# Kernel tuning notes

Hardware: AMD Instinct MI355X
Metric: run time of the kernel (lower is better)

The kernel has to match this reference:

```python
import jax, jax.numpy as jnp
import numpy as np

EMBED = 1024

def setup_inputs() -> dict:
    key = jax.random.key(0)
    ks = jax.random.split(key, 7)
    s = 1.0 / np.sqrt(EMBED)
    x = jax.random.normal(ks[0], (8, 2048, EMBED), dtype=jnp.float32)
    Wk = jax.random.uniform(ks[1], (EMBED, EMBED), jnp.float32, -s, s)
    bk = jax.random.uniform(ks[2], (EMBED,), jnp.float32, -s, s)
    Wq = jax.random.uniform(ks[3], (EMBED, EMBED), jnp.float32, -s, s)
    bq = jax.random.uniform(ks[4], (EMBED,), jnp.float32, -s, s)
    Wv = jax.random.uniform(ks[5], (EMBED, EMBED), jnp.float32, -s, s)
    bv = jax.random.uniform(ks[6], (EMBED,), jnp.float32, -s, s)
    return {"x": x, "Wq": Wq, "bq": bq, "Wk": Wk, "bk": bk, "Wv": Wv, "bv": bv}

def reference(x, Wq, bq, Wk, bk, Wv, bv):
    # Linear projections (PyTorch Linear: y = x @ W^T + b; W here stored as [in, out] = W^T)
    Q = x @ Wq + bq          # [b, s, d]
    K = x @ Wk + bk
    V = x @ Wv + bv
    scale = 1.0 / jnp.sqrt(jnp.asarray(x.shape[-1], x.dtype))
    scores = jnp.einsum('bqd,bkd->bqk', Q, K) * scale  # [b, s, s]
    attn = jax.nn.softmax(scores, axis=-1)
    return jnp.einsum('bqk,bkd->bqd', attn, V)
```

## Files before the change

### kernel.cpp

```cpp
#include <hip/hip_runtime.h>

typedef __attribute__((ext_vector_type(4))) float f32x4;
typedef __attribute__((ext_vector_type(8))) short bf16x8;
typedef __attribute__((ext_vector_type(4))) unsigned short u16x4;

static __device__ __forceinline__ unsigned short f2bf(float f) {
    union { float f; unsigned int u; } a; a.f = f;
    unsigned int u = a.u;
    unsigned int r = (u + 0x7FFFu + ((u >> 16) & 1u)) >> 16;
    return (unsigned short)r;
}
static __device__ __forceinline__ float bf2f(unsigned short h) {
    union { unsigned int u; float f; } a; a.u = ((unsigned int)h) << 16;
    return a.f;
}
static __device__ __forceinline__ unsigned lds_off(const void* p) {
    return (unsigned)(unsigned long long)(const __attribute__((address_space(3))) void*)p;
}

__global__ __launch_bounds__(256) void cvt_f32_bf16(const float* __restrict__ in,
                                                    unsigned short* __restrict__ out) {
    long long i = ((long long)blockIdx.x * 256 + threadIdx.x) * 4;
    float4 f = *(const float4*)(in + i);
    u16x4 u;
    u[0] = f2bf(f.x); u[1] = f2bf(f.y); u[2] = f2bf(f.z); u[3] = f2bf(f.w);
    *(u16x4*)(out + i) = u;
}

__global__ __launch_bounds__(256) void transpose_w(const float* __restrict__ W0,
                                                   const float* __restrict__ W1,
                                                   const float* __restrict__ W2,
                                                   unsigned short* __restrict__ Wt) {
    __shared__ float t[32][33];
    int mat = blockIdx.z;
    const float* W = (mat == 0) ? W0 : (mat == 1) ? W1 : W2;
    unsigned short* out = Wt + (long long)mat * 1024 * 1024;
    int n0 = blockIdx.x * 32, k0 = blockIdx.y * 32;
    int tx = threadIdx.x, ty = threadIdx.y;
#pragma unroll
    for (int q = 0; q < 4; ++q)
        t[ty + 8 * q][tx] = W[(long long)(k0 + ty + 8 * q) * 1024 + n0 + tx];
    __syncthreads();
#pragma unroll
    for (int q = 0; q < 4; ++q)
        out[(long long)(n0 + ty + 8 * q) * 1024 + k0 + tx] = f2bf(t[tx][ty + 8 * q]);
}

#define GBM 256
#define GBN 256
#define GBK 64

template<int OUT_MODE, int BIAS_MODE>
__global__ __launch_bounds__(512, 2) void gemm8p(
    const unsigned short* __restrict__ A, int lda, long long strideA,
    const unsigned short* __restrict__ B, int ldb, long long strideB,
    void* __restrict__ Cv, int ldc, long long strideC,
    const float* __restrict__ bias, int K, float scale)
{
    __shared__ __align__(16) unsigned short As[2][GBM * GBK];
    __shared__ __align__(16) unsigned short Bs[2][GBN * GBK];

    const int gx = gridDim.x, gy = gridDim.y;
    int lin = blockIdx.x + gx * (blockIdx.y + gy * blockIdx.z);
    const int nwg = gx * gy * gridDim.z;
    const int qch = nwg >> 3;
    int swz = (lin & 7) * qch + (lin >> 3);
    const int bx = swz % gx; int t2 = swz / gx;
    const int by = t2 % gy;  const int bz = t2 / gy;

    const unsigned short* Ag = A + (long long)bz * strideA;
    const unsigned short* Bg = B + (long long)bz * strideB;
    const int m0 = by * GBM, n0 = bx * GBN;

    const int tid  = threadIdx.x;
    const int lane = tid & 63, w = tid >> 6;
    const int wm = w >> 2, wn = w & 3;
    const int l15 = lane & 15, l4 = lane >> 4;

    const int sg = (lane & 7) ^ ((lane >> 3) & 7);
    const unsigned short* Asrc = Ag + (long long)(m0 + w * 8 + (lane >> 3)) * lda + sg * 8;
    const unsigned short* Bsrc = Bg + (long long)(n0 + w * 8 + (lane >> 3)) * ldb + sg * 8;

    f32x4 acc[8][4] = {};

    auto issueA = [&](int p, int kt, int l) {
        __builtin_amdgcn_global_load_lds(
            (const __attribute__((address_space(1))) void*)(Asrc + (long long)(l * 64) * lda + kt),
            (__attribute__((address_space(3))) void*)(&As[p][(l * 64 + w * 8) * GBK]), 16, 0, 0);
    };
    auto issueB = [&](int p, int kt, int l) {
        __builtin_amdgcn_global_load_lds(
            (const __attribute__((address_space(1))) void*)(Bsrc + (long long)(l * 64) * ldb + kt),
            (__attribute__((address_space(3))) void*)(&Bs[p][(l * 64 + w * 8) * GBK]), 16, 0, 0);
    };
    auto readA = [&](bf16x8 (&af)[4], int p, int mh, int ks) {
#pragma unroll
        for (int fi = 0; fi < 4; ++fi) {
            int ar = wm * 128 + mh * 64 + fi * 16 + l15;
            int slot = (ks * 4 + l4) ^ (ar & 7);
            unsigned off = lds_off(&As[p][ar * GBK + slot * 8]);
            asm volatile("ds_read_b128 %0, %1" : "=v"(af[fi]) : "v"(off));
        }
    };
    auto readB = [&](bf16x8 (&bf)[4], int p, int ks) {
#pragma unroll
        for (int nj = 0; nj < 4; ++nj) {
            int br = wn * 64 + nj * 16 + l15;
            int slot = (ks * 4 + l4) ^ (br & 7);
            unsigned off = lds_off(&Bs[p][br * GBK + slot * 8]);
            asm volatile("ds_read_b128 %0, %1" : "=v"(bf[nj]) : "v"(off));
        }
    };
    auto mfma16 = [&](int mh, bf16x8 (&af)[4], bf16x8 (&bf)[4]) {
#pragma unroll
        for (int fi = 0; fi < 4; ++fi)
#pragma unroll
            for (int nj = 0; nj < 4; ++nj)
                acc[mh * 4 + fi][nj] = __builtin_amdgcn_mfma_f32_16x16x32_bf16(
                    af[fi], bf[nj], acc[mh * 4 + fi][nj], 0, 0, 0);
    };

#define VMCNT2 asm volatile("s_waitcnt vmcnt(2)" ::: "memory")
#define VMCNT0 asm volatile("s_waitcnt vmcnt(0)" ::: "memory")
#define LGKM0  asm volatile("s_waitcnt lgkmcnt(0)" ::: "memory")
#define SCHED0 __builtin_amdgcn_sched_barrier(0)
#define BARR   __builtin_amdgcn_s_barrier()
#define PRIO1  __builtin_amdgcn_s_setprio(1)
#define PRIO0  __builtin_amdgcn_s_setprio(0)

    issueB(0, 0, 0); issueB(0, 0, 1); issueB(0, 0, 2); issueB(0, 0, 3);
    issueA(0, 0, 0); issueA(0, 0, 2); issueA(0, 0, 1); issueA(0, 0, 3);

    const int NT = K >> 6;
    bf16x8 a0[4], a1[4], b0[4], b1[4];

    for (int t = 0; t < NT - 1; ++t) {
        const int p = t & 1, q = p ^ 1;
        const int kn = (t + 1) << 6;
        VMCNT2; BARR; SCHED0;
        issueB(q, kn, 0); issueB(q, kn, 1);
        readA(a0, p, 0, 0); readB(b0, p, 0);
        LGKM0; SCHED0; PRIO1; mfma16(0, a0, b0); PRIO0;
        VMCNT2; BARR; SCHED0;
        issueB(q, kn, 2); issueB(q, kn, 3);
        readA(a1, p, 1, 0);
        LGKM0; SCHED0; PRIO1; mfma16(1, a1, b0); PRIO0;
        issueA(q, kn, 0); issueA(q, kn, 2);
        readA(a0, p, 0, 1); readB(b1, p, 1);
        LGKM0; SCHED0; PRIO1; mfma16(0, a0, b1); PRIO0;
        issueA(q, kn, 1); issueA(q, kn, 3);
        readA(a1, p, 1, 1);
        LGKM0; SCHED0; PRIO1; mfma16(1, a1, b1); PRIO0;
    }
    {
        const int p = (NT - 1) & 1;
        VMCNT0; BARR; SCHED0;
        readA(a0, p, 0, 0); readB(b0, p, 0);
        LGKM0; SCHED0; PRIO1; mfma16(0, a0, b0); PRIO0;
        readA(a1, p, 1, 0);
        LGKM0; SCHED0; PRIO1; mfma16(1, a1, b0); PRIO0;
        readA(a0, p, 0, 1); readB(b1, p, 1);
        LGKM0; SCHED0; PRIO1; mfma16(0, a0, b1); PRIO0;
        readA(a1, p, 1, 1);
        LGKM0; SCHED0; PRIO1; mfma16(1, a1, b1); PRIO0;
    }

    const float* bias_v = bias;
    asm volatile("" : "+s"(bias_v));
    unsigned short* Cb = (unsigned short*)Cv;
    float* Cf = (float*)Cv;
    long long cbase = (long long)bz * strideC;
#pragma unroll
    for (int mh = 0; mh < 2; ++mh)
#pragma unroll
    for (int fi = 0; fi < 4; ++fi) {
#pragma unroll
        for (int nj = 0; nj < 4; ++nj) {
            int n = n0 + wn * 64 + nj * 16 + l15;
            float bn = (BIAS_MODE == 1) ? bias_v[n] : 0.0f;
#pragma unroll
            for (int r = 0; r < 4; ++r) {
                int m = m0 + wm * 128 + mh * 64 + fi * 16 + l4 * 4 + r;
                float v = acc[mh * 4 + fi][nj][r] * scale + bn;
                if (BIAS_MODE == 2) v += bias_v[m];
                long long idx = cbase + (long long)m * ldc + n;
                if (OUT_MODE == 0) Cb[idx] = f2bf(v);
                else               Cf[idx] = v;
            }
        }
    }
}

__global__ __launch_bounds__(256) void softmax_rows_bf16(unsigned short* __restrict__ S) {
    int row  = blockIdx.x * 4 + (threadIdx.x >> 6);
    int lane = threadIdx.x & 63;
    unsigned short* Srow = S + (long long)row * 2048;
    float v[32];
    float mx = -1e30f;
#pragma unroll
    for (int j = 0; j < 4; ++j) {
        bf16x8 h = *(const bf16x8*)(Srow + j * 512 + lane * 8);
#pragma unroll
        for (int e = 0; e < 8; ++e) {
            float f = bf2f((unsigned short)h[e]);
            v[j * 8 + e] = f;
            mx = fmaxf(mx, f);
        }
    }
#pragma unroll
    for (int o = 32; o; o >>= 1) mx = fmaxf(mx, __shfl_xor(mx, o));
    float sum = 0.0f;
#pragma unroll
    for (int e = 0; e < 32; ++e) {
        v[e] = __expf(v[e] - mx);
        sum += v[e];
    }
#pragma unroll
    for (int o = 32; o; o >>= 1) sum += __shfl_xor(sum, o);
    float inv = 1.0f / sum;
#pragma unroll
    for (int j = 0; j < 4; ++j) {
        bf16x8 h;
#pragma unroll
        for (int e = 0; e < 8; ++e) h[e] = (short)f2bf(v[j * 8 + e] * inv);
        *(bf16x8*)(Srow + j * 512 + lane * 8) = h;
    }
}

extern "C" void kernel_launch(void* const* d_in, const int* in_sizes, int n_in,
                              void* d_out, int out_size, void* d_ws, size_t ws_size,
                              hipStream_t stream) {
    (void)in_sizes; (void)n_in; (void)out_size; (void)ws_size;
    const float* x  = (const float*)d_in[0];
    const float* Wq = (const float*)d_in[1];
    const float* bq = (const float*)d_in[2];
    const float* Wk = (const float*)d_in[3];
    const float* bk = (const float*)d_in[4];
    const float* Wv = (const float*)d_in[5];
    const float* bv = (const float*)d_in[6];

    char* ws = (char*)d_ws;
    unsigned short* Wt  = (unsigned short*)ws;
    unsigned short* Qb  = (unsigned short*)(ws + 6291456);
    unsigned short* Kb  = (unsigned short*)(ws + 39845888);
    unsigned short* Vt  = (unsigned short*)(ws + 73400320);
    unsigned short* xb  = (unsigned short*)(ws + 106954752);
    unsigned short* Sb  = (unsigned short*)(ws + 106954752);

    cvt_f32_bf16<<<dim3(16384), dim3(256), 0, stream>>>(x, xb);
    transpose_w<<<dim3(32, 32, 3), dim3(32, 8), 0, stream>>>(Wq, Wk, Wv, Wt);

    gemm8p<0, 1><<<dim3(4, 64, 1), dim3(512), 0, stream>>>(
        xb, 1024, 0, Wt, 1024, 0, Qb, 1024, 0, bq, 1024, 1.0f);
    gemm8p<0, 1><<<dim3(4, 64, 1), dim3(512), 0, stream>>>(
        xb, 1024, 0, Wt + 1048576, 1024, 0, Kb, 1024, 0, bk, 1024, 1.0f);
    gemm8p<0, 2><<<dim3(64, 4, 1), dim3(512), 0, stream>>>(
        Wt + 2097152, 1024, 0, xb, 1024, 0, Vt, 16384, 0, bv, 1024, 1.0f);

    gemm8p<0, 0><<<dim3(8, 8, 8), dim3(512), 0, stream>>>(
        Qb, 1024, 2097152LL, Kb, 1024, 2097152LL,
        Sb, 2048, 4194304LL, nullptr, 1024, 0.03125f);

    softmax_rows_bf16<<<dim3(4096), dim3(256), 0, stream>>>(Sb);

    gemm8p<1, 0><<<dim3(4, 8, 8), dim3(512), 0, stream>>>(
        Sb, 2048, 4194304LL,
        Vt, 16384, 2048LL,
        d_out, 1024, 2097152LL, nullptr, 2048, 1.0f);
}
```

Baseline: 269.7 us.

## Switch GEMM to 4-stage K=32 LDS ring buffer with deeper prefetch

Replaces the double-buffered K=64 tile pipeline with a four-slot ring of K=32 tiles in a single 128KB LDS array, keeping three tiles in flight ahead of compute. The swizzle changes to a 4-slot XOR pattern and LDS read addresses are precomputed as constant offsets, which cuts per-read address arithmetic. The aim is to hide global-load latency better and cut barrier stalls. In exchange there are twice as many barriers per K, and 128KB of LDS per block may limit occupancy to fewer blocks than the launch bound of two.

Result: slower. 288.2 us (+6.9%).

```diff
diff --git a/kernel.cpp b/kernel.cpp
--- a/kernel.cpp
+++ b/kernel.cpp
@@ -48,17 +48,15 @@
 
 #define GBM 256
 #define GBN 256
-#define GBK 64
 
 template<int OUT_MODE, int BIAS_MODE>
-__global__ __launch_bounds__(512, 2) void gemm8p(
+__global__ __launch_bounds__(512, 2) void gemm4b(
     const unsigned short* __restrict__ A, int lda, long long strideA,
     const unsigned short* __restrict__ B, int ldb, long long strideB,
     void* __restrict__ Cv, int ldc, long long strideC,
     const float* __restrict__ bias, int K, float scale)
 {
-    __shared__ __align__(16) unsigned short As[2][GBM * GBK];
-    __shared__ __align__(16) unsigned short Bs[2][GBN * GBK];
+    __shared__ __align__(16) char lds[131072];
 
     const int gx = gridDim.x, gy = gridDim.y;
     int lin = blockIdx.x + gx * (blockIdx.y + gy * blockIdx.z);
@@ -77,37 +75,41 @@
     const int wm = w >> 2, wn = w & 3;
     const int l15 = lane & 15, l4 = lane >> 4;
 
-    const int sg = (lane & 7) ^ ((lane >> 3) & 7);
-    const unsigned short* Asrc = Ag + (long long)(m0 + w * 8 + (lane >> 3)) * lda + sg * 8;
-    const unsigned short* Bsrc = Bg + (long long)(n0 + w * 8 + (lane >> 3)) * ldb + sg * 8;
+    const int lr  = lane >> 2;
+    const int lsl = (lane & 3) ^ (lr & 3);
+    const unsigned short* Asrc = Ag + (long long)(m0 + w * 16 + lr) * lda + lsl * 8;
+    const unsigned short* Bsrc = Bg + (long long)(n0 + w * 16 + lr) * ldb + lsl * 8;
 
     f32x4 acc[8][4] = {};
 
-    auto issueA = [&](int p, int kt, int l) {
+    auto issueA = [&](int wb, int kt, int l) {
         __builtin_amdgcn_global_load_lds(
-            (const __attribute__((address_space(1))) void*)(Asrc + (long long)(l * 64) * lda + kt),
-            (__attribute__((address_space(3))) void*)(&As[p][(l * 64 + w * 8) * GBK]), 16, 0, 0);
-    };
-    auto issueB = [&](int p, int kt, int l) {
+            (const __attribute__((address_space(1))) void*)(Asrc + (long long)(l * 128) * lda + kt),
+            (__attribute__((address_space(3))) void*)(lds + wb + (l * 128 + w * 16) * 64), 16, 0, 0);
+    };
+    auto issueB = [&](int wb, int kt, int l) {
         __builtin_amdgcn_global_load_lds(
-            (const __attribute__((address_space(1))) void*)(Bsrc + (long long)(l * 64) * ldb + kt),
-            (__attribute__((address_space(3))) void*)(&Bs[p][(l * 64 + w * 8) * GBK]), 16, 0, 0);
-    };
-    auto readA = [&](bf16x8 (&af)[4], int p, int mh, int ks) {
+            (const __attribute__((address_space(1))) void*)(Bsrc + (long long)(l * 128) * ldb + kt),
+            (__attribute__((address_space(3))) void*)(lds + 65536 + wb + (l * 128 + w * 16) * 64), 16, 0, 0);
+    };
+
+    const unsigned ldsb  = lds_off(lds);
+    const unsigned slotb = (unsigned)((l4 ^ (l15 & 3)) * 16);
+    const unsigned aoffc = ldsb + (unsigned)((wm * 128 + l15) * 64) + slotb;
+    const unsigned boffc = ldsb + 65536u + (unsigned)((wn * 64 + l15) * 64) + slotb;
+
+    bf16x8 a0[4], a1[4], b0[4];
+    auto readA = [&](bf16x8 (&af)[4], int rb, int mh) {
 #pragma unroll
         for (int fi = 0; fi < 4; ++fi) {
-            int ar = wm * 128 + mh * 64 + fi * 16 + l15;
-            int slot = (ks * 4 + l4) ^ (ar & 7);
-            unsigned off = lds_off(&As[p][ar * GBK + slot * 8]);
+            unsigned off = aoffc + rb + mh * 4096 + fi * 1024;
             asm volatile("ds_read_b128 %0, %1" : "=v"(af[fi]) : "v"(off));
         }
     };
-    auto readB = [&](bf16x8 (&bf)[4], int p, int ks) {
+    auto readB = [&](bf16x8 (&bf)[4], int rb) {
 #pragma unroll
         for (int nj = 0; nj < 4; ++nj) {
-            int br = wn * 64 + nj * 16 + l15;
-            int slot = (ks * 4 + l4) ^ (br & 7);
-            unsigned off = lds_off(&Bs[p][br * GBK + slot * 8]);
+            unsigned off = boffc + rb + nj * 1024;
             asm volatile("ds_read_b128 %0, %1" : "=v"(bf[nj]) : "v"(off));
         }
     };
@@ -120,7 +122,8 @@
                     af[fi], bf[nj], acc[mh * 4 + fi][nj], 0, 0, 0);
     };
 
-#define VMCNT2 asm volatile("s_waitcnt vmcnt(2)" ::: "memory")
+#define VMCNT8 asm volatile("s_waitcnt vmcnt(8)" ::: "memory")
+#define VMCNT4 asm volatile("s_waitcnt vmcnt(4)" ::: "memory")
 #define VMCNT0 asm volatile("s_waitcnt vmcnt(0)" ::: "memory")
 #define LGKM0  asm volatile("s_waitcnt lgkmcnt(0)" ::: "memory")
 #define SCHED0 __builtin_amdgcn_sched_barrier(0)
@@ -128,41 +131,42 @@
 #define PRIO1  __builtin_amdgcn_s_setprio(1)
 #define PRIO0  __builtin_amdgcn_s_setprio(0)
 
-    issueB(0, 0, 0); issueB(0, 0, 1); issueB(0, 0, 2); issueB(0, 0, 3);
-    issueA(0, 0, 0); issueA(0, 0, 2); issueA(0, 0, 1); issueA(0, 0, 3);
-
-    const int NT = K >> 6;
-    bf16x8 a0[4], a1[4], b0[4], b1[4];
-
-    for (int t = 0; t < NT - 1; ++t) {
-        const int p = t & 1, q = p ^ 1;
-        const int kn = (t + 1) << 6;
-        VMCNT2; BARR; SCHED0;
-        issueB(q, kn, 0); issueB(q, kn, 1);
-        readA(a0, p, 0, 0); readB(b0, p, 0);
+    const int NT = K >> 5;
+#pragma unroll
+    for (int t = 0; t < 3; ++t) {
+        int wb = t * 16384, kt = t * 32;
+        issueA(wb, kt, 0); issueA(wb, kt, 1);
+        issueB(wb, kt, 0); issueB(wb, kt, 1);
+    }
+
+    int rb = 0;
+    for (int t = 0; t < NT - 2; ++t) {
+        VMCNT8; BARR; SCHED0;
+        const int kt3 = (t + 3) * 32;
+        const int wb = (rb + 49152) & 65535;
+        const bool more = (t + 3) < NT;
+        if (more) { issueA(wb, kt3, 0); issueA(wb, kt3, 1); }
+        readB(b0, rb); readA(a0, rb, 0);
         LGKM0; SCHED0; PRIO1; mfma16(0, a0, b0); PRIO0;
-        VMCNT2; BARR; SCHED0;
-        issueB(q, kn, 2); issueB(q, kn, 3);
-        readA(a1, p, 1, 0);
+        if (more) { issueB(wb, kt3, 0); issueB(wb, kt3, 1); }
+        readA(a1, rb, 1);
         LGKM0; SCHED0; PRIO1; mfma16(1, a1, b0); PRIO0;
-        issueA(q, kn, 0); issueA(q, kn, 2);
-        readA(a0, p, 0, 1); readB(b1, p, 1);
-        LGKM0; SCHED0; PRIO1; mfma16(0, a0, b1); PRIO0;
-        issueA(q, kn, 1); issueA(q, kn, 3);
-        readA(a1, p, 1, 1);
-        LGKM0; SCHED0; PRIO1; mfma16(1, a1, b1); PRIO0;
+        rb = (rb + 16384) & 65535;
     }
     {
-        const int p = (NT - 1) & 1;
+        VMCNT4; BARR; SCHED0;
+        readB(b0, rb); readA(a0, rb, 0);
+        LGKM0; SCHED0; PRIO1; mfma16(0, a0, b0); PRIO0;
+        readA(a1, rb, 1);
+        LGKM0; SCHED0; PRIO1; mfma16(1, a1, b0); PRIO0;
+        rb = (rb + 16384) & 65535;
+    }
+    {
         VMCNT0; BARR; SCHED0;
-        readA(a0, p, 0, 0); readB(b0, p, 0);
+        readB(b0, rb); readA(a0, rb, 0);
         LGKM0; SCHED0; PRIO1; mfma16(0, a0, b0); PRIO0;
-        readA(a1, p, 1, 0);
+        readA(a1, rb, 1);
         LGKM0; SCHED0; PRIO1; mfma16(1, a1, b0); PRIO0;
-        readA(a0, p, 0, 1); readB(b1, p, 1);
-        LGKM0; SCHED0; PRIO1; mfma16(0, a0, b1); PRIO0;
-        readA(a1, p, 1, 1);
-        LGKM0; SCHED0; PRIO1; mfma16(1, a1, b1); PRIO0;
     }
 
     const float* bias_v = bias;
@@ -250,20 +254,20 @@
     cvt_f32_bf16<<<dim3(16384), dim3(256), 0, stream>>>(x, xb);
     transpose_w<<<dim3(32, 32, 3), dim3(32, 8), 0, stream>>>(Wq, Wk, Wv, Wt);
 
-    gemm8p<0, 1><<<dim3(4, 64, 1), dim3(512), 0, stream>>>(
+    gemm4b<0, 1><<<dim3(4, 64, 1), dim3(512), 0, stream>>>(
         xb, 1024, 0, Wt, 1024, 0, Qb, 1024, 0, bq, 1024, 1.0f);
-    gemm8p<0, 1><<<dim3(4, 64, 1), dim3(512), 0, stream>>>(
+    gemm4b<0, 1><<<dim3(4, 64, 1), dim3(512), 0, stream>>>(
         xb, 1024, 0, Wt + 1048576, 1024, 0, Kb, 1024, 0, bk, 1024, 1.0f);
-    gemm8p<0, 2><<<dim3(64, 4, 1), dim3(512), 0, stream>>>(
+    gemm4b<0, 2><<<dim3(64, 4, 1), dim3(512), 0, stream>>>(
         Wt + 2097152, 1024, 0, xb, 1024, 0, Vt, 16384, 0, bv, 1024, 1.0f);
 
-    gemm8p<0, 0><<<dim3(8, 8, 8), dim3(512), 0, stream>>>(
+    gemm4b<0, 0><<<dim3(8, 8, 8), dim3(512), 0, stream>>>(
         Qb, 1024, 2097152LL, Kb, 1024, 2097152LL,
         Sb, 2048, 4194304LL, nullptr, 1024, 0.03125f);
 
     softmax_rows_bf16<<<dim3(4096), dim3(256), 0, stream>>>(Sb);
 
-    gemm8p<1, 0><<<dim3(4, 8, 8), dim3(512), 0, stream>>>(
+    gemm4b<1, 0><<<dim3(4, 8, 8), dim3(512), 0, stream>>>(
         Sb, 2048, 4194304LL,
         Vt, 16384, 2048LL,
         d_out, 1024, 2097152LL, nullptr, 2048, 1.0f);
```

## Restructure GEMM main loop into half-tile staged prefetch with per-phase barriers

Applied to the files above, without the earlier changes.

Replaces the separate A/B shared arrays with one raw LDS buffer and precomputes swizzled read offsets so each LDS read is a base plus a constant stride. The K-loop is reorganized so each MFMA phase is bracketed by barriers and the next tile's A/B halves are staged in finer pieces, with the first A half of tile t+2 prefetched into the buffer being consumed. The peeled epilogue iteration is folded in via guards. The goal is better overlap of global-to-LDS loads with MFMA work and cheaper address arithmetic, at the cost of many more barriers per iteration and tighter buffer-reuse hazards.

New measurement: 285.8 us. 1.06x slower.

```diff
diff --git a/kernel.cpp b/kernel.cpp
--- a/kernel.cpp
+++ b/kernel.cpp
@@ -48,7 +48,6 @@
 
 #define GBM 256
 #define GBN 256
-#define GBK 64
 
 template<int OUT_MODE, int BIAS_MODE>
 __global__ __launch_bounds__(512, 2) void gemm8p(
@@ -57,8 +56,7 @@
     void* __restrict__ Cv, int ldc, long long strideC,
     const float* __restrict__ bias, int K, float scale)
 {
-    __shared__ __align__(16) unsigned short As[2][GBM * GBK];
-    __shared__ __align__(16) unsigned short Bs[2][GBN * GBK];
+    __shared__ __align__(16) char lds[131072];
 
     const int gx = gridDim.x, gy = gridDim.y;
     int lin = blockIdx.x + gx * (blockIdx.y + gy * blockIdx.z);
@@ -77,37 +75,48 @@
     const int wm = w >> 2, wn = w & 3;
     const int l15 = lane & 15, l4 = lane >> 4;
 
-    const int sg = (lane & 7) ^ ((lane >> 3) & 7);
-    const unsigned short* Asrc = Ag + (long long)(m0 + w * 8 + (lane >> 3)) * lda + sg * 8;
-    const unsigned short* Bsrc = Bg + (long long)(n0 + w * 8 + (lane >> 3)) * ldb + sg * 8;
+    const int sr = lane >> 3;
+    const int ss = (lane & 7) ^ sr;
+    const unsigned short* Asrc = Ag + (long long)(m0 + w * 8 + sr) * lda + ss * 8;
+    const unsigned short* Bsrc = Bg + (long long)(n0 + w * 8 + sr) * ldb + ss * 8;
 
     f32x4 acc[8][4] = {};
 
-    auto issueA = [&](int p, int kt, int l) {
-        __builtin_amdgcn_global_load_lds(
-            (const __attribute__((address_space(1))) void*)(Asrc + (long long)(l * 64) * lda + kt),
-            (__attribute__((address_space(3))) void*)(&As[p][(l * 64 + w * 8) * GBK]), 16, 0, 0);
-    };
-    auto issueB = [&](int p, int kt, int l) {
-        __builtin_amdgcn_global_load_lds(
-            (const __attribute__((address_space(1))) void*)(Bsrc + (long long)(l * 64) * ldb + kt),
-            (__attribute__((address_space(3))) void*)(&Bs[p][(l * 64 + w * 8) * GBK]), 16, 0, 0);
-    };
+    auto stageA = [&](int p, int kt, int h) {
+#pragma unroll
+        for (int i = 0; i < 2; ++i)
+            __builtin_amdgcn_global_load_lds(
+                (const __attribute__((address_space(1))) void*)(Asrc + (long long)(h * 128 + i * 64) * lda + kt),
+                (__attribute__((address_space(3))) void*)(lds + p * 32768 + (h * 128 + i * 64 + w * 8) * 128), 16, 0, 0);
+    };
+    auto stageB = [&](int p, int kt, int h) {
+#pragma unroll
+        for (int i = 0; i < 2; ++i)
+            __builtin_amdgcn_global_load_lds(
+                (const __attribute__((address_space(1))) void*)(Bsrc + (long long)(h * 128 + i * 64) * ldb + kt),
+                (__attribute__((address_space(3))) void*)(lds + 65536 + p * 32768 + (h * 128 + i * 64 + w * 8) * 128), 16, 0, 0);
+    };
+
+    const unsigned ldsb = lds_off(lds);
+    const unsigned as0  = (unsigned)(((l4    ) ^ (l15 & 7)) * 16);
+    const unsigned as1  = (unsigned)(((l4 + 4) ^ (l15 & 7)) * 16);
+    const unsigned aRow = (unsigned)((wm * 128 + l15) * 128);
+    const unsigned bRow = (unsigned)((wn * 64 + l15) * 128);
+
+    bf16x8 a0[4], a1[4], b0[4], b1[4];
     auto readA = [&](bf16x8 (&af)[4], int p, int mh, int ks) {
+        unsigned base = ldsb + (unsigned)(p * 32768) + aRow + (unsigned)(mh * 8192) + (ks ? as1 : as0);
 #pragma unroll
         for (int fi = 0; fi < 4; ++fi) {
-            int ar = wm * 128 + mh * 64 + fi * 16 + l15;
-            int slot = (ks * 4 + l4) ^ (ar & 7);
-            unsigned off = lds_off(&As[p][ar * GBK + slot * 8]);
+            unsigned off = base + (unsigned)(fi * 2048);
             asm volatile("ds_read_b128 %0, %1" : "=v"(af[fi]) : "v"(off));
         }
     };
     auto readB = [&](bf16x8 (&bf)[4], int p, int ks) {
+        unsigned base = ldsb + 65536u + (unsigned)(p * 32768) + bRow + (ks ? as1 : as0);
 #pragma unroll
         for (int nj = 0; nj < 4; ++nj) {
-            int br = wn * 64 + nj * 16 + l15;
-            int slot = (ks * 4 + l4) ^ (br & 7);
-            unsigned off = lds_off(&Bs[p][br * GBK + slot * 8]);
+            unsigned off = base + (unsigned)(nj * 2048);
             asm volatile("ds_read_b128 %0, %1" : "=v"(bf[nj]) : "v"(off));
         }
     };
@@ -128,41 +137,28 @@
 #define PRIO1  __builtin_amdgcn_s_setprio(1)
 #define PRIO0  __builtin_amdgcn_s_setprio(0)
 
-    issueB(0, 0, 0); issueB(0, 0, 1); issueB(0, 0, 2); issueB(0, 0, 3);
-    issueA(0, 0, 0); issueA(0, 0, 2); issueA(0, 0, 1); issueA(0, 0, 3);
-
     const int NT = K >> 6;
-    bf16x8 a0[4], a1[4], b0[4], b1[4];
-
-    for (int t = 0; t < NT - 1; ++t) {
+    stageA(0, 0, 0); stageA(0, 0, 1); stageB(0, 0, 0); stageB(0, 0, 1);
+    stageA(1, 64, 0);
+    VMCNT2; BARR; SCHED0;
+
+    for (int t = 0; t < NT; ++t) {
         const int p = t & 1, q = p ^ 1;
-        const int kn = (t + 1) << 6;
-        VMCNT2; BARR; SCHED0;
-        issueB(q, kn, 0); issueB(q, kn, 1);
+        const int kt1 = (t + 1) << 6, kt2 = (t + 2) << 6;
+        const bool s1 = (t + 1) < NT, s2 = (t + 2) < NT;
         readA(a0, p, 0, 0); readB(b0, p, 0);
-        LGKM0; SCHED0; PRIO1; mfma16(0, a0, b0); PRIO0;
-        VMCNT2; BARR; SCHED0;
-        issueB(q, kn, 2); issueB(q, kn, 3);
+        if (s1) stageB(q, kt1, 0);
+        BARR; LGKM0; SCHED0; PRIO1; mfma16(0, a0, b0); PRIO0; BARR;
         readA(a1, p, 1, 0);
-        LGKM0; SCHED0; PRIO1; mfma16(1, a1, b0); PRIO0;
-        issueA(q, kn, 0); issueA(q, kn, 2);
+        if (s1) stageA(q, kt1, 1);
+        BARR; LGKM0; SCHED0; PRIO1; mfma16(1, a1, b0); PRIO0; BARR;
         readA(a0, p, 0, 1); readB(b1, p, 1);
-        LGKM0; SCHED0; PRIO1; mfma16(0, a0, b1); PRIO0;
-        issueA(q, kn, 1); issueA(q, kn, 3);
+        if (s1) stageB(q, kt1, 1);
+        BARR; LGKM0; SCHED0; PRIO1; mfma16(0, a0, b1); PRIO0; BARR;
         readA(a1, p, 1, 1);
-        LGKM0; SCHED0; PRIO1; mfma16(1, a1, b1); PRIO0;
-    }
-    {
-        const int p = (NT - 1) & 1;
-        VMCNT0; BARR; SCHED0;
-        readA(a0, p, 0, 0); readB(b0, p, 0);
-        LGKM0; SCHED0; PRIO1; mfma16(0, a0, b0); PRIO0;
-        readA(a1, p, 1, 0);
-        LGKM0; SCHED0; PRIO1; mfma16(1, a1, b0); PRIO0;
-        readA(a0, p, 0, 1); readB(b1, p, 1);
-        LGKM0; SCHED0; PRIO1; mfma16(0, a0, b1); PRIO0;
-        readA(a1, p, 1, 1);
-        LGKM0; SCHED0; PRIO1; mfma16(1, a1, b1); PRIO0;
+        if (s2) stageA(p, kt2, 0);
+        if (t == NT - 1) { VMCNT0; } else { VMCNT2; }
+        BARR; LGKM0; SCHED0; PRIO1; mfma16(1, a1, b1); PRIO0; BARR;
     }
 
     const float* bias_v = bias;
```
